# Performance work log

Hardware: AMD Instinct MI355X
Metric: run time of the kernel (lower is better)

## Reference

```python
import jax, jax.numpy as jnp
import numpy as np

N, A, K, B, P, HW = 8, 16368, 200, 20, 4, 128
ALPHA = 1.0   # cfg.loss_cls_alpha (undefined global in source; assume 1.0)
EPS = 1e-7


def _bce(p, y):
    # elementwise binary cross entropy on probabilities, clamped like torch BCELoss
    p = jnp.clip(p, EPS, 1.0 - EPS)
    return -(y * jnp.log(p) + (1.0 - y) * jnp.log1p(-p))


def _smooth_l1(d):
    ad = jnp.abs(d)
    return jnp.where(ad < 1.0, 0.5 * d * d, ad - 0.5)


def setup_inputs() -> dict:
    key = jax.random.key(0)
    ks = jax.random.split(key, 11)
    map_class = jax.random.uniform(ks[0], (N, A), minval=0.01, maxval=0.99)
    map_box = jax.random.normal(ks[1], (N, A, 4))
    map_coef = jax.random.normal(ks[2], (N, A, P)) * 0.5
    proto = jax.random.normal(ks[3], (N, P, HW, HW))
    anchor_center = jax.random.uniform(ks[4], (A, 2)) * 128.0          # (ch, cw)
    anchor_hw = jax.random.uniform(ks[5], (A, 2)) * 100.0 + 24.0       # (h, w) > 0
    gt_boxes = jax.random.uniform(ks[6], (N, B, 4)) * 60.0 + 4.0       # (ch, cw, h, w) > 0
    gt_masks = jax.random.uniform(ks[7], (N, B, HW, HW))
    pos_idx = jax.random.randint(ks[8], (N, K), 0, A)
    neg_idx = jax.random.randint(ks[9], (N, 3 * K), 0, A)
    gt_idx = jax.random.randint(ks[10], (N, K), 0, B)
    return dict(map_class=map_class, map_box=map_box, map_coef=map_coef, proto=proto,
                anchor_center=anchor_center, anchor_hw=anchor_hw,
                gt_boxes=gt_boxes, gt_masks=gt_masks,
                pos_idx=pos_idx, neg_idx=neg_idx, gt_idx=gt_idx)


def reference(map_class, map_box, map_coef, proto, anchor_center, anchor_hw,
              gt_boxes, gt_masks, pos_idx, neg_idx, gt_idx):
    k = jnp.asarray(K, map_class.dtype)
    # ---- classification (positives vs ones, sampled negatives vs zeros) ----
    p_pos = jnp.take_along_axis(map_class, pos_idx, axis=1)            # [N,K]
    p_neg = jnp.take_along_axis(map_class, neg_idx, axis=1)           # [N,3K]
    loss_cls_pos = _bce(p_pos, 1.0).mean(axis=1)                       # [N]
    loss_cls_neg = _bce(p_neg, 0.0).mean(axis=1)                       # [N]
    # ---- localization: SmoothL1 per coord against encoded GT offsets ----
    pr = jnp.take_along_axis(map_box, pos_idx[..., None], axis=1)      # [N,K,4]
    ac = anchor_center[pos_idx]                                        # [N,K,2]
    ahw = anchor_hw[pos_idx]                                           # [N,K,2]
    gt = jnp.take_along_axis(gt_boxes, gt_idx[..., None], axis=1)      # [N,K,4]
    t_ch = (gt[..., 0] - ac[..., 0]) / ahw[..., 0]
    t_cw = (gt[..., 1] - ac[..., 1]) / ahw[..., 1]
    t_h = jnp.log10(gt[..., 2] / ahw[..., 0])
    t_w = jnp.log10(gt[..., 3] / ahw[..., 1])
    tgt = jnp.stack([t_ch, t_cw, t_h, t_w], axis=-1)                   # [N,K,4]
    loss_loc = _smooth_l1(pr - tgt).sum(axis=(1, 2))                   # [N] (each per-coord loss is a 1-elem mean)
    # ---- mask: sigmoid(coef . proto) vs GT mask (already 128x128) ----
    coef = jnp.take_along_axis(map_coef, pos_idx[..., None], axis=1)   # [N,K,P]
    pred = jax.nn.sigmoid(jnp.einsum('nkp,nphw->nkhw', coef, proto))   # [N,K,HW,HW]
    goal = jnp.take_along_axis(gt_masks, gt_idx[:, :, None, None], axis=1)  # [N,K,HW,HW]
    loss_msk = _bce(pred, goal).mean(axis=(2, 3)).sum(axis=1)          # [N]
    # ---- per-image normalization by num matched anchors, mean over batch ----
    per_img = (loss_cls_pos + loss_cls_neg) / k + ALPHA * loss_loc / k + loss_msk / k
    return per_img.mean()
```

## Files before the change

### kernel.cpp

```cpp
#include <hip/hip_runtime.h>
#include <cstddef>

#define NN   8
#define AA   16368
#define KK   200
#define BB   20
#define PP   4
#define HW2  16384
#define KCH  4
#define KPC  (KK / KCH)

#define LOG2E 1.44269504088896340736f
#define LN2   0.69314718055994530942f

__device__ __forceinline__ float block_reduce_sum(float v) {
    #pragma unroll
    for (int o = 32; o > 0; o >>= 1) v += __shfl_down(v, o, 64);
    __shared__ float s[4];
    const int lane = threadIdx.x & 63;
    const int wid  = threadIdx.x >> 6;
    if (lane == 0) s[wid] = v;
    __syncthreads();
    float r = 0.f;
    if (threadIdx.x == 0) r = s[0] + s[1] + s[2] + s[3];
    return r;
}

__device__ __forceinline__ float smooth_l1(float d) {
    float ad = fabsf(d);
    return (ad < 1.f) ? 0.5f * d * d : ad - 0.5f;
}

__global__ void zero_out_kernel(float* out) { out[0] = 0.f; }

__global__ __launch_bounds__(256) void fused_loss_kernel(
        const float* __restrict__ map_class,
        const float* __restrict__ map_box,
        const float* __restrict__ map_coef,
        const float* __restrict__ proto,
        const float* __restrict__ anchor_center,
        const float* __restrict__ anchor_hw,
        const float* __restrict__ gt_boxes,
        const float* __restrict__ gt_masks,
        const int*   __restrict__ pos_idx,
        const int*   __restrict__ neg_idx,
        const int*   __restrict__ gt_idx,
        float* __restrict__ out) {
    const int blk = blockIdx.x;
    const int tid = threadIdx.x;

    if (blk >= KCH * 128) {
        const int n = blk - KCH * 128;
        const float EPSF = 1e-7f;
        const float W_CLSPOS = 1.0f / ((float)NN * (float)KK * (float)KK);
        const float W_CLSNEG = 1.0f / ((float)NN * 3.0f * (float)KK * (float)KK);
        const float W_LOC    = 1.0f / ((float)NN * (float)KK);
        const float LOG10E   = 0.43429448190325176f;

        float acc = 0.f;
        for (int k = tid; k < KK; k += 256) {
            const int a = pos_idx[n * KK + k];
            const int b = gt_idx[n * KK + k];
            float p = map_class[(size_t)n * AA + a];
            p = fminf(fmaxf(p, EPSF), 1.f - EPSF);
            acc += (-__logf(p)) * W_CLSPOS;

            const float ach = anchor_center[a * 2 + 0];
            const float acw = anchor_center[a * 2 + 1];
            const float ah  = anchor_hw[a * 2 + 0];
            const float aw  = anchor_hw[a * 2 + 1];
            const float* g  = gt_boxes + ((size_t)n * BB + b) * 4;
            const float t0 = (g[0] - ach) / ah;
            const float t1 = (g[1] - acw) / aw;
            const float t2 = __logf(g[2] / ah) * LOG10E;
            const float t3 = __logf(g[3] / aw) * LOG10E;
            const float* pr = map_box + ((size_t)n * AA + a) * 4;
            acc += (smooth_l1(pr[0] - t0) + smooth_l1(pr[1] - t1)
                  + smooth_l1(pr[2] - t2) + smooth_l1(pr[3] - t3)) * W_LOC;
        }
        for (int j = tid; j < 3 * KK; j += 256) {
            const int a = neg_idx[n * 3 * KK + j];
            float p = map_class[(size_t)n * AA + a];
            p = fminf(fmaxf(p, EPSF), 1.f - EPSF);
            acc += (-__logf(1.f - p)) * W_CLSNEG;
        }
        float tot = block_reduce_sum(acc);
        if (tid == 0) atomicAdd(out, tot);
        return;
    }

    const int kc = blk >> 7;
    const int pc = blk & 127;
    const int n  = pc >> 4;
    const int ch = pc & 15;

    __shared__ float4 sC[KPC];
    __shared__ float  S[BB][4];

    if (kc == 0) {
        if (tid < BB * 4) ((float*)S)[tid] = 0.f;
        __syncthreads();
        if (tid < KK) {
            const int a = pos_idx[n * KK + tid];
            const float4 c = *(const float4*)(map_coef + ((size_t)n * AA + a) * 4);
            if (tid < KPC) {
                float4 cl;
                cl.x = c.x * LOG2E; cl.y = c.y * LOG2E;
                cl.z = c.z * LOG2E; cl.w = c.w * LOG2E;
                sC[tid] = cl;
            }
            const int b = gt_idx[n * KK + tid];
            atomicAdd(&S[b][0], c.x); atomicAdd(&S[b][1], c.y);
            atomicAdd(&S[b][2], c.z); atomicAdd(&S[b][3], c.w);
        }
    } else {
        if (tid < KPC) {
            const int a = pos_idx[n * KK + kc * KPC + tid];
            const float4 c = *(const float4*)(map_coef + ((size_t)n * AA + a) * 4);
            float4 cl;
            cl.x = c.x * LOG2E; cl.y = c.y * LOG2E;
            cl.z = c.z * LOG2E; cl.w = c.w * LOG2E;
            sC[tid] = cl;
        }
    }
    __syncthreads();

    const int vidx = ch * 256 + tid;
    const float4* pr = (const float4*)(proto + (size_t)n * PP * HW2);
    const float4 p0 = pr[0 * (HW2 / 4) + vidx];
    const float4 p1 = pr[1 * (HW2 / 4) + vidx];
    const float4 p2 = pr[2 * (HW2 / 4) + vidx];
    const float4 p3 = pr[3 * (HW2 / 4) + vidx];

    float corr0 = 0.f, corr1 = 0.f, corr2 = 0.f, corr3 = 0.f;
    if (kc == 0) {
        const float4* gm = (const float4*)(gt_masks + (size_t)n * BB * HW2);
        float ax0=0,ax1=0,ax2=0,ax3=0, ay0=0,ay1=0,ay2=0,ay3=0;
        float az0=0,az1=0,az2=0,az3=0, aw0=0,aw1=0,aw2=0,aw3=0;
        #pragma unroll
        for (int b = 0; b < BB; ++b) {
            const float4 y = gm[(size_t)b * (HW2 / 4) + vidx];
            const float s0 = S[b][0], s1 = S[b][1], s2 = S[b][2], s3 = S[b][3];
            ax0 = fmaf(y.x, s0, ax0); ay0 = fmaf(y.x, s1, ay0);
            az0 = fmaf(y.x, s2, az0); aw0 = fmaf(y.x, s3, aw0);
            ax1 = fmaf(y.y, s0, ax1); ay1 = fmaf(y.y, s1, ay1);
            az1 = fmaf(y.y, s2, az1); aw1 = fmaf(y.y, s3, aw1);
            ax2 = fmaf(y.z, s0, ax2); ay2 = fmaf(y.z, s1, ay2);
            az2 = fmaf(y.z, s2, az2); aw2 = fmaf(y.z, s3, aw2);
            ax3 = fmaf(y.w, s0, ax3); ay3 = fmaf(y.w, s1, ay3);
            az3 = fmaf(y.w, s2, az3); aw3 = fmaf(y.w, s3, aw3);
        }
        corr0 = fmaf(ax0, p0.x, fmaf(ay0, p1.x, fmaf(az0, p2.x, aw0 * p3.x)));
        corr1 = fmaf(ax1, p0.y, fmaf(ay1, p1.y, fmaf(az1, p2.y, aw1 * p3.y)));
        corr2 = fmaf(ax2, p0.z, fmaf(ay2, p1.z, fmaf(az2, p2.z, aw2 * p3.z)));
        corr3 = fmaf(ax3, p0.w, fmaf(ay3, p1.w, fmaf(az3, p2.w, aw3 * p3.w)));
    }

    float sl0 = 0.f, sl1 = 0.f, sl2 = 0.f, sl3 = 0.f;
    #pragma unroll 2
    for (int k = 0; k < KPC; ++k) {
        const float4 c = sC[k];
        const float z0 = fmaf(c.x, p0.x, fmaf(c.y, p1.x, fmaf(c.z, p2.x, c.w * p3.x)));
        const float z1 = fmaf(c.x, p0.y, fmaf(c.y, p1.y, fmaf(c.z, p2.y, c.w * p3.y)));
        const float z2 = fmaf(c.x, p0.z, fmaf(c.y, p1.z, fmaf(c.z, p2.z, c.w * p3.z)));
        const float z3 = fmaf(c.x, p0.w, fmaf(c.y, p1.w, fmaf(c.z, p2.w, c.w * p3.w)));
        sl0 += fmaxf(z0, 0.f) + __log2f(1.f + __builtin_amdgcn_exp2f(-fabsf(z0)));
        sl1 += fmaxf(z1, 0.f) + __log2f(1.f + __builtin_amdgcn_exp2f(-fabsf(z1)));
        sl2 += fmaxf(z2, 0.f) + __log2f(1.f + __builtin_amdgcn_exp2f(-fabsf(z2)));
        sl3 += fmaxf(z3, 0.f) + __log2f(1.f + __builtin_amdgcn_exp2f(-fabsf(z3)));
    }

    const float v = LN2 * (sl0 + sl1 + sl2 + sl3) - (corr0 + corr1 + corr2 + corr3);
    float tot = block_reduce_sum(v);
    if (tid == 0) {
        const float W_MSK = 1.0f / ((float)NN * (float)KK * (float)HW2);
        atomicAdd(out, tot * W_MSK);
    }
}

extern "C" void kernel_launch(void* const* d_in, const int* in_sizes, int n_in,
                              void* d_out, int out_size, void* d_ws, size_t ws_size,
                              hipStream_t stream) {
    const float* map_class     = (const float*)d_in[0];
    const float* map_box       = (const float*)d_in[1];
    const float* map_coef      = (const float*)d_in[2];
    const float* proto         = (const float*)d_in[3];
    const float* anchor_center = (const float*)d_in[4];
    const float* anchor_hw     = (const float*)d_in[5];
    const float* gt_boxes      = (const float*)d_in[6];
    const float* gt_masks      = (const float*)d_in[7];
    const int*   pos_idx       = (const int*)d_in[8];
    const int*   neg_idx       = (const int*)d_in[9];
    const int*   gt_idx        = (const int*)d_in[10];
    float* out = (float*)d_out;

    zero_out_kernel<<<1, 1, 0, stream>>>(out);
    fused_loss_kernel<<<KCH * 128 + NN, 256, 0, stream>>>(
        map_class, map_box, map_coef, proto, anchor_center, anchor_hw,
        gt_boxes, gt_masks, pos_idx, neg_idx, gt_idx, out);
}
```

Baseline: 97.38 us.

## Replace per-element log2 with running products and spread GT-mask correction across chunks

The softplus sum is rewritten so each element contributes an exp2 folded into a running product, with a single log2 per lane at the end. relu(z) is recovered as 0.5*(z+|z|), and the sum of z comes from the coefficient sum dotted with proto. The GT-mask correlation work, which only the kc==0 blocks did before, is now split so each k-chunk block handles BB/KCH boxes, which evens out the load. Multiplying up to 50 factors in (1,2] can reach about 2^50 and still fits in fp32 range, but rounding error now builds up in the product.

After: 97.91 us. About the same (+0.5%).

```diff
diff --git a/kernel.cpp b/kernel.cpp
--- a/kernel.cpp
+++ b/kernel.cpp
@@ -9,6 +9,7 @@
 #define HW2  16384
 #define KCH  4
 #define KPC  (KK / KCH)
+#define BPB  (BB / KCH)
 
 #define LOG2E 1.44269504088896340736f
 #define LN2   0.69314718055994530942f
@@ -89,56 +90,57 @@
         return;
     }
 
-    const int kc = blk >> 7;
-    const int pc = blk & 127;
-    const int n  = pc >> 4;
-    const int ch = pc & 15;
+    const int kc  = blk >> 7;
+    const int pc  = blk & 127;
+    const int n   = pc >> 4;
+    const int ch  = pc & 15;
+    const int bLo = kc * BPB;
+
+    const int vidx = ch * 256 + tid;
+    const float4* prp = (const float4*)(proto + (size_t)n * PP * HW2);
+    const float4 p0 = prp[0 * (HW2 / 4) + vidx];
+    const float4 p1 = prp[1 * (HW2 / 4) + vidx];
+    const float4 p2 = prp[2 * (HW2 / 4) + vidx];
+    const float4 p3 = prp[3 * (HW2 / 4) + vidx];
 
     __shared__ float4 sC[KPC];
-    __shared__ float  S[BB][4];
-
-    if (kc == 0) {
-        if (tid < BB * 4) ((float*)S)[tid] = 0.f;
-        __syncthreads();
-        if (tid < KK) {
-            const int a = pos_idx[n * KK + tid];
-            const float4 c = *(const float4*)(map_coef + ((size_t)n * AA + a) * 4);
-            if (tid < KPC) {
-                float4 cl;
-                cl.x = c.x * LOG2E; cl.y = c.y * LOG2E;
-                cl.z = c.z * LOG2E; cl.w = c.w * LOG2E;
-                sC[tid] = cl;
-            }
-            const int b = gt_idx[n * KK + tid];
-            atomicAdd(&S[b][0], c.x); atomicAdd(&S[b][1], c.y);
-            atomicAdd(&S[b][2], c.z); atomicAdd(&S[b][3], c.w);
-        }
-    } else {
-        if (tid < KPC) {
-            const int a = pos_idx[n * KK + kc * KPC + tid];
-            const float4 c = *(const float4*)(map_coef + ((size_t)n * AA + a) * 4);
+    __shared__ float  S[BPB][4];
+    __shared__ float  Cs[4];
+
+    if (tid < BPB * 4 + 4) {
+        if (tid < BPB * 4) ((float*)S)[tid] = 0.f;
+        else               Cs[tid - BPB * 4] = 0.f;
+    }
+    __syncthreads();
+
+    if (tid < KK) {
+        const int a = pos_idx[n * KK + tid];
+        const int b = gt_idx[n * KK + tid];
+        const float4 c = *(const float4*)(map_coef + ((size_t)n * AA + a) * 4);
+        const int bl = b - bLo;
+        if (bl >= 0 && bl < BPB) {
+            atomicAdd(&S[bl][0], c.x); atomicAdd(&S[bl][1], c.y);
+            atomicAdd(&S[bl][2], c.z); atomicAdd(&S[bl][3], c.w);
+        }
+        const int kl = tid - kc * KPC;
+        if (kl >= 0 && kl < KPC) {
             float4 cl;
             cl.x = c.x * LOG2E; cl.y = c.y * LOG2E;
             cl.z = c.z * LOG2E; cl.w = c.w * LOG2E;
-            sC[tid] = cl;
+            sC[kl] = cl;
+            atomicAdd(&Cs[0], cl.x); atomicAdd(&Cs[1], cl.y);
+            atomicAdd(&Cs[2], cl.z); atomicAdd(&Cs[3], cl.w);
         }
     }
     __syncthreads();
 
-    const int vidx = ch * 256 + tid;
-    const float4* pr = (const float4*)(proto + (size_t)n * PP * HW2);
-    const float4 p0 = pr[0 * (HW2 / 4) + vidx];
-    const float4 p1 = pr[1 * (HW2 / 4) + vidx];
-    const float4 p2 = pr[2 * (HW2 / 4) + vidx];
-    const float4 p3 = pr[3 * (HW2 / 4) + vidx];
-
-    float corr0 = 0.f, corr1 = 0.f, corr2 = 0.f, corr3 = 0.f;
-    if (kc == 0) {
-        const float4* gm = (const float4*)(gt_masks + (size_t)n * BB * HW2);
+    float corr;
+    {
+        const float4* gm = (const float4*)(gt_masks + ((size_t)n * BB + bLo) * HW2);
         float ax0=0,ax1=0,ax2=0,ax3=0, ay0=0,ay1=0,ay2=0,ay3=0;
         float az0=0,az1=0,az2=0,az3=0, aw0=0,aw1=0,aw2=0,aw3=0;
         #pragma unroll
-        for (int b = 0; b < BB; ++b) {
+        for (int b = 0; b < BPB; ++b) {
             const float4 y = gm[(size_t)b * (HW2 / 4) + vidx];
             const float s0 = S[b][0], s1 = S[b][1], s2 = S[b][2], s3 = S[b][3];
             ax0 = fmaf(y.x, s0, ax0); ay0 = fmaf(y.x, s1, ay0);
@@ -150,27 +152,43 @@
             ax3 = fmaf(y.w, s0, ax3); ay3 = fmaf(y.w, s1, ay3);
             az3 = fmaf(y.w, s2, az3); aw3 = fmaf(y.w, s3, aw3);
         }
-        corr0 = fmaf(ax0, p0.x, fmaf(ay0, p1.x, fmaf(az0, p2.x, aw0 * p3.x)));
-        corr1 = fmaf(ax1, p0.y, fmaf(ay1, p1.y, fmaf(az1, p2.y, aw1 * p3.y)));
-        corr2 = fmaf(ax2, p0.z, fmaf(ay2, p1.z, fmaf(az2, p2.z, aw2 * p3.z)));
-        corr3 = fmaf(ax3, p0.w, fmaf(ay3, p1.w, fmaf(az3, p2.w, aw3 * p3.w)));
-    }
-
-    float sl0 = 0.f, sl1 = 0.f, sl2 = 0.f, sl3 = 0.f;
-    #pragma unroll 2
+        const float c0 = fmaf(ax0, p0.x, fmaf(ay0, p1.x, fmaf(az0, p2.x, aw0 * p3.x)));
+        const float c1 = fmaf(ax1, p0.y, fmaf(ay1, p1.y, fmaf(az1, p2.y, aw1 * p3.y)));
+        const float c2 = fmaf(ax2, p0.z, fmaf(ay2, p1.z, fmaf(az2, p2.z, aw2 * p3.z)));
+        const float c3 = fmaf(ax3, p0.w, fmaf(ay3, p1.w, fmaf(az3, p2.w, aw3 * p3.w)));
+        corr = (c0 + c1) + (c2 + c3);
+    }
+
+    float prod0 = 1.f, prod1 = 1.f, prod2 = 1.f, prod3 = 1.f;
+    float sab0 = 0.f, sab1 = 0.f, sab2 = 0.f, sab3 = 0.f;
+    #pragma unroll 5
     for (int k = 0; k < KPC; ++k) {
         const float4 c = sC[k];
         const float z0 = fmaf(c.x, p0.x, fmaf(c.y, p1.x, fmaf(c.z, p2.x, c.w * p3.x)));
         const float z1 = fmaf(c.x, p0.y, fmaf(c.y, p1.y, fmaf(c.z, p2.y, c.w * p3.y)));
         const float z2 = fmaf(c.x, p0.z, fmaf(c.y, p1.z, fmaf(c.z, p2.z, c.w * p3.z)));
         const float z3 = fmaf(c.x, p0.w, fmaf(c.y, p1.w, fmaf(c.z, p2.w, c.w * p3.w)));
-        sl0 += fmaxf(z0, 0.f) + __log2f(1.f + __builtin_amdgcn_exp2f(-fabsf(z0)));
-        sl1 += fmaxf(z1, 0.f) + __log2f(1.f + __builtin_amdgcn_exp2f(-fabsf(z1)));
-        sl2 += fmaxf(z2, 0.f) + __log2f(1.f + __builtin_amdgcn_exp2f(-fabsf(z2)));
-        sl3 += fmaxf(z3, 0.f) + __log2f(1.f + __builtin_amdgcn_exp2f(-fabsf(z3)));
-    }
-
-    const float v = LN2 * (sl0 + sl1 + sl2 + sl3) - (corr0 + corr1 + corr2 + corr3);
+        const float a0 = fabsf(z0), a1 = fabsf(z1), a2 = fabsf(z2), a3 = fabsf(z3);
+        sab0 += a0; sab1 += a1; sab2 += a2; sab3 += a3;
+        const float x0 = __builtin_amdgcn_exp2f(-a0);
+        const float x1 = __builtin_amdgcn_exp2f(-a1);
+        const float x2 = __builtin_amdgcn_exp2f(-a2);
+        const float x3 = __builtin_amdgcn_exp2f(-a3);
+        prod0 = fmaf(prod0, x0, prod0);
+        prod1 = fmaf(prod1, x1, prod1);
+        prod2 = fmaf(prod2, x2, prod2);
+        prod3 = fmaf(prod3, x3, prod3);
+    }
+
+    const float csx = Cs[0], csy = Cs[1], csz = Cs[2], csw = Cs[3];
+    const float m0 = fmaf(csx, p0.x, fmaf(csy, p1.x, fmaf(csz, p2.x, csw * p3.x)));
+    const float m1 = fmaf(csx, p0.y, fmaf(csy, p1.y, fmaf(csz, p2.y, csw * p3.y)));
+    const float m2 = fmaf(csx, p0.z, fmaf(csy, p1.z, fmaf(csz, p2.z, csw * p3.z)));
+    const float m3 = fmaf(csx, p0.w, fmaf(csy, p1.w, fmaf(csz, p2.w, csw * p3.w)));
+    const float sl = 0.5f * (((m0 + sab0) + (m1 + sab1)) + ((m2 + sab2) + (m3 + sab3)))
+                   + ((__log2f(prod0) + __log2f(prod1)) + (__log2f(prod2) + __log2f(prod3)));
+
+    const float v = LN2 * sl - corr;
     float tot = block_reduce_sum(v);
     if (tid == 0) {
         const float W_MSK = 1.0f / ((float)NN * (float)KK * (float)HW2);
```
